# Kernel tuning notes

Measured on AMD Instinct MI355X. Metric: run time of the kernel, lower is better.

## Reference

```python
import jax, jax.numpy as jnp
import numpy as np

N_NODES = 100000
N_EDGES = 3200000
IN_FEAT = 64
OUT_FEAT = 64
NUM_RELS = 16


def setup_inputs() -> dict:
    key = jax.random.key(0)
    k1, k2, k3, k4, k5, k6 = jax.random.split(key, 6)
    h = jax.random.normal(k1, (N_NODES, IN_FEAT), dtype=jnp.float32)
    weight = jax.random.normal(k2, (NUM_RELS, IN_FEAT, OUT_FEAT), dtype=jnp.float32) * 0.1
    norm = jax.random.uniform(k3, (N_EDGES, 1), dtype=jnp.float32)
    src = jax.random.randint(k4, (N_EDGES,), 0, N_NODES, dtype=jnp.int32)
    dst = jax.random.randint(k5, (N_EDGES,), 0, N_NODES, dtype=jnp.int32)
    rel_type = jax.random.randint(k6, (N_EDGES,), 0, NUM_RELS, dtype=jnp.int32)
    return {"h": h, "weight": weight, "norm": norm, "src": src, "dst": dst, "rel_type": rel_type}


def reference(h, weight, norm, src, dst, rel_type):
    # RGCN layer (use_edge_nn=False, num_bases==num_rels, no bias, activation=relu).
    # torch: msg_e = (h[src_e] @ weight[rel_e]) * norm_e ; h_v = relu(sum_{e->v} msg_e)
    # Efficient form: transform every node under every relation once (R is small),
    # then gather per-edge instead of gathering [E, in, out] weight slices.
    n_nodes = h.shape[0]
    transformed = jnp.einsum('nd,rdo->nro', h, weight)          # [N, R, out]
    msg = transformed[src, rel_type] * norm                      # [E, out]
    agg = jax.ops.segment_sum(msg, dst, num_segments=n_nodes)    # [N, out]
    return jax.nn.relu(agg)                                      # dropout is identity in eval
```

## Files before the change

kernel.cpp:

```cpp
#include <hip/hip_runtime.h>

#define N_NODES 100000
#define N_EDGES 3200000
#define FEAT 64
#define NUM_RELS 16
#define CAP 64
#define OVF_CAP 32768
#define RANGES_W 4
#define NODES_PER_W 25000
#define FILL_BLOCKS 1024
#define AGG_BLOCKS (NODES_PER_W / 4)

typedef float f32x4 __attribute__((ext_vector_type(4)));
typedef float f32x16 __attribute__((ext_vector_type(16)));
typedef short s16x8 __attribute__((ext_vector_type(8)));
typedef int   i32x2 __attribute__((ext_vector_type(2)));
typedef int   i32x4 __attribute__((ext_vector_type(4)));

__device__ __forceinline__ unsigned short f32_to_bf16_rne(float x) {
    unsigned int u = __float_as_uint(x);
    unsigned int r = (u + 0x7fffu + ((u >> 16) & 1u)) >> 16;
    return (unsigned short)r;
}
__device__ __forceinline__ float bf16_to_f32(unsigned short s) {
    return __uint_as_float(((unsigned int)s) << 16);
}
__device__ __forceinline__ int t_offset(int s, int r) {
    return ((s >> 4) << 14) | (r << 10) | ((s & 15) << 6);
}

__global__ __launch_bounds__(256) void cvt_h_kernel(const float4* __restrict__ h4,
                                                    ushort4* __restrict__ hb4, int n4)
{
    int i = blockIdx.x * 256 + threadIdx.x;
    if (i < n4) {
        float4 v = h4[i];
        ushort4 o;
        o.x = f32_to_bf16_rne(v.x); o.y = f32_to_bf16_rne(v.y);
        o.z = f32_to_bf16_rne(v.z); o.w = f32_to_bf16_rne(v.w);
        hb4[i] = o;
    }
}

__global__ __launch_bounds__(256) void cvt_w_kernel(const float* __restrict__ W,
                                                    unsigned short* __restrict__ Wt)
{
    int t = blockIdx.x * 256 + threadIdx.x;
    int r = t >> 12, o = (t >> 6) & 63, k = t & 63;
    Wt[t] = f32_to_bf16_rne(W[(r << 12) + (k << 6) + o]);
}

__global__ __launch_bounds__(256) void gemm_T_kernel(
    const unsigned short* __restrict__ hb,
    const unsigned short* __restrict__ Wt,
    unsigned short* __restrict__ T)
{
    __shared__ short lds[4][16][68];
    const int lane  = threadIdx.x & 63;
    const int w     = threadIdx.x >> 6;
    const int row0  = blockIdx.x * 64 + w * 16;
    if (row0 >= N_NODES) return;
    const int q     = lane & 15;
    const int g4    = lane >> 4;

    const unsigned short* ap = hb + ((size_t)(row0 + q) << 6) + (g4 << 3);
    const s16x8 a0 = *reinterpret_cast<const s16x8*>(ap);
    const s16x8 a1 = *reinterpret_cast<const s16x8*>(ap + 32);

    const unsigned short* wbase = Wt + ((size_t)q << 6) + (g4 << 3);
    unsigned short* tb = T + ((size_t)(row0 >> 4) << 14);
    const int nrd = lane >> 4;
    const int c   = lane & 15;

    auto loadB = [&](s16x8* Bf, int r) {
        const unsigned short* wp = wbase + ((size_t)r << 12);
        #pragma unroll
        for (int t = 0; t < 4; ++t)
            #pragma unroll
            for (int kh = 0; kh < 2; ++kh)
                Bf[t * 2 + kh] = *reinterpret_cast<const s16x8*>(wp + (t << 10) + (kh << 5));
    };
    auto compStore = [&](const s16x8* Bf, int rr) {
        f32x4 acc[4] = {f32x4{0,0,0,0}, f32x4{0,0,0,0}, f32x4{0,0,0,0}, f32x4{0,0,0,0}};
        #pragma unroll
        for (int t = 0; t < 4; ++t) {
            acc[t] = __builtin_amdgcn_mfma_f32_16x16x32_bf16(Bf[t*2+0], a0, acc[t], 0, 0, 0);
            acc[t] = __builtin_amdgcn_mfma_f32_16x16x32_bf16(Bf[t*2+1], a1, acc[t], 0, 0, 0);
        }
        #pragma unroll
        for (int t = 0; t < 4; ++t) {
            i32x2 pk;
            pk.x = (int)((unsigned)f32_to_bf16_rne(acc[t][0]) |
                         ((unsigned)f32_to_bf16_rne(acc[t][1]) << 16));
            pk.y = (int)((unsigned)f32_to_bf16_rne(acc[t][2]) |
                         ((unsigned)f32_to_bf16_rne(acc[t][3]) << 16));
            *reinterpret_cast<i32x2*>(&lds[w][q][g4 * 4 + t * 16]) = pk;
        }
        asm volatile("s_waitcnt lgkmcnt(0)" ::: "memory");
        unsigned short* tr = tb + (rr << 10);
        #pragma unroll
        for (int j = 0; j < 4; ++j) {
            const int n = nrd + 4 * j;
            i32x2 v = *reinterpret_cast<const i32x2*>(&lds[w][n][c * 4]);
            *reinterpret_cast<i32x2*>(tr + (n << 6) + (c << 2)) = v;
        }
    };

    s16x8 B0[8], B1[8];
    loadB(B0, 0);
    #pragma unroll
    for (int rp = 0; rp < 16; rp += 2) {
        loadB(B1, rp + 1);
        compStore(B0, rp);
        if (rp + 2 < 16) loadB(B0, rp + 2);
        compStore(B1, rp + 1);
    }
}

__global__ __launch_bounds__(256) void fill_agg_kernel(
    const int* __restrict__ src, const int* __restrict__ dst,
    const int* __restrict__ rel, const float* __restrict__ norm,
    int* __restrict__ cnt, int* __restrict__ ovfc, i32x4* __restrict__ ovf,
    i32x2* __restrict__ payF, const i32x2* __restrict__ payG,
    const unsigned short* __restrict__ T, float* __restrict__ out,
    int fillRange, int aggRange)
{
    const int nFill = (fillRange >= 0) ? FILL_BLOCKS : 0;
    if ((int)blockIdx.x < nFill) {
        const int lo = fillRange * NODES_PER_W, hi = lo + NODES_PER_W;
        for (int e = blockIdx.x * 256 + threadIdx.x; e < N_EDGES; e += nFill * 256) {
            int d = __builtin_nontemporal_load(&dst[e]);
            if (d >= lo && d < hi) {
                int s   = __builtin_nontemporal_load(&src[e]);
                int rl  = __builtin_nontemporal_load(&rel[e]);
                float nv = __builtin_nontemporal_load(&norm[e]);
                int tofs = t_offset(s, rl);
                int pos = atomicAdd(&cnt[d], 1);
                if (pos < CAP) {
                    i32x2 p; p.x = tofs; p.y = __float_as_int(nv);
                    payF[(size_t)(d - lo) * CAP + pos] = p;
                } else {
                    int op = atomicAdd(ovfc, 1);
                    if (op < OVF_CAP) {
                        i32x4 o; o.x = d; o.y = tofs;
                        o.z = __float_as_int(nv); o.w = 0;
                        ovf[op] = o;
                    }
                }
            }
        }
    } else {
        const int b    = blockIdx.x - nFill;
        const int lo   = aggRange * NODES_PER_W;
        const int lane = threadIdx.x & 63;
        const int d    = lo + b * 4 + (threadIdx.x >> 6);

        const int degRaw = __builtin_amdgcn_readfirstlane(cnt[d]);
        const int deg    = min(degRaw, CAP);
        const i32x2* pp  = payG + (size_t)(d - lo) * CAP;

        float acc = 0.f;
        int i = 0;
        for (; i + 4 <= deg; i += 4) {
            i32x2 p0 = __builtin_nontemporal_load(&pp[i]);
            i32x2 p1 = __builtin_nontemporal_load(&pp[i + 1]);
            i32x2 p2 = __builtin_nontemporal_load(&pp[i + 2]);
            i32x2 p3 = __builtin_nontemporal_load(&pp[i + 3]);
            const unsigned short t0 = T[(size_t)(unsigned)p0.x + lane];
            const unsigned short t1 = T[(size_t)(unsigned)p1.x + lane];
            const unsigned short t2 = T[(size_t)(unsigned)p2.x + lane];
            const unsigned short t3 = T[(size_t)(unsigned)p3.x + lane];
            acc = fmaf(__int_as_float(p0.y), bf16_to_f32(t0), acc);
            acc = fmaf(__int_as_float(p1.y), bf16_to_f32(t1), acc);
            acc = fmaf(__int_as_float(p2.y), bf16_to_f32(t2), acc);
            acc = fmaf(__int_as_float(p3.y), bf16_to_f32(t3), acc);
        }
        for (; i < deg; ++i) {
            i32x2 p = __builtin_nontemporal_load(&pp[i]);
            const unsigned short t = T[(size_t)(unsigned)p.x + lane];
            acc = fmaf(__int_as_float(p.y), bf16_to_f32(t), acc);
        }
        if (degRaw > CAP) {
            const int no = min(__builtin_amdgcn_readfirstlane(*ovfc), OVF_CAP);
            for (int j = 0; j < no; ++j) {
                i32x4 o = ovf[j];
                if (o.x == d) {
                    const unsigned short t = T[(size_t)(unsigned)o.y + lane];
                    acc = fmaf(__int_as_float(o.z), bf16_to_f32(t), acc);
                }
            }
        }
        out[((size_t)d << 6) + lane] = fmaxf(acc, 0.f);
    }
}

__global__ __launch_bounds__(256) void rgcn_edge_kernel(
    const float* __restrict__ h, const float* __restrict__ W,
    const float* __restrict__ norm, const int* __restrict__ src,
    const int* __restrict__ dst, const int* __restrict__ rel,
    float* __restrict__ out)
{
    const int lane = threadIdx.x & 63;
    const int w    = threadIdx.x >> 6;
    const int r    = blockIdx.x & 15;
    const int inst = blockIdx.x >> 4;
    const int wavesPerRel = (gridDim.x >> 4) * 4;
    const int wi   = inst * 4 + w;

    float wreg[64];
    const float* Wr = W + (size_t)r * (FEAT * FEAT) + lane;
    #pragma unroll
    for (int d = 0; d < 64; ++d) wreg[d] = Wr[d * 64];

    const int nChunks = N_EDGES / 64;
    for (int c = wi; c < nChunks; c += wavesPerRel) {
        const int base = c * 64;
        unsigned long long m = __ballot(rel[base + lane] == r);
        while (m) {
            const int idx = __ffsll(m) - 1;
            m &= (m - 1);
            const int e = base + idx;
            const int se = __builtin_amdgcn_readfirstlane(src[e]);
            const int de = __builtin_amdgcn_readfirstlane(dst[e]);
            const float nv = __uint_as_float(
                __builtin_amdgcn_readfirstlane(__float_as_uint(norm[e])));
            const float* hp = h + ((size_t)se << 6);
            f32x16 ha, hb2, hc, hd;
            asm volatile(
                "s_load_dwordx16 %0, %4, 0x0\n\ts_load_dwordx16 %1, %4, 0x40\n\t"
                "s_load_dwordx16 %2, %4, 0x80\n\ts_load_dwordx16 %3, %4, 0xc0\n\t"
                "s_waitcnt lgkmcnt(0)"
                : "=&s"(ha), "=&s"(hb2), "=&s"(hc), "=&s"(hd) : "s"(hp));
            float a0 = 0.f, a1 = 0.f, a2 = 0.f, a3 = 0.f;
            #pragma unroll
            for (int j = 0; j < 16; ++j) {
                a0 = fmaf(ha[j], wreg[j], a0);       a1 = fmaf(hb2[j], wreg[16 + j], a1);
                a2 = fmaf(hc[j], wreg[32 + j], a2);  a3 = fmaf(hd[j], wreg[48 + j], a3);
            }
            unsafeAtomicAdd(&out[(size_t)de * FEAT + lane], ((a0 + a1) + (a2 + a3)) * nv);
        }
    }
}

__global__ __launch_bounds__(256) void relu_kernel(float4* __restrict__ out, int n4)
{
    int i = blockIdx.x * 256 + threadIdx.x;
    if (i < n4) {
        float4 v = out[i];
        v.x = fmaxf(v.x, 0.f); v.y = fmaxf(v.y, 0.f);
        v.z = fmaxf(v.z, 0.f); v.w = fmaxf(v.w, 0.f);
        out[i] = v;
    }
}

static inline size_t align256(size_t x) { return (x + 255) & ~(size_t)255; }

extern "C" void kernel_launch(void* const* d_in, const int* in_sizes, int n_in,
                              void* d_out, int out_size, void* d_ws, size_t ws_size,
                              hipStream_t stream)
{
    (void)in_sizes; (void)n_in;

    const float* h    = (const float*)d_in[0];
    const float* W    = (const float*)d_in[1];
    const float* norm = (const float*)d_in[2];
    const int*   src  = (const int*)d_in[3];
    const int*   dst  = (const int*)d_in[4];
    const int*   rel  = (const int*)d_in[5];
    float*       out  = (float*)d_out;

    const size_t szT    = (size_t)N_NODES * NUM_RELS * FEAT * 2;
    const size_t szHb   = (size_t)N_NODES * FEAT * 2;
    const size_t szWt   = (size_t)NUM_RELS * FEAT * FEAT * 2;
    const size_t szCnt  = (size_t)N_NODES * 4;
    const size_t szPayW = (size_t)NODES_PER_W * CAP * 8;
    const size_t szOvf  = (size_t)OVF_CAP * 16;

    const size_t needWin = align256(szT) + align256(szHb) + align256(szWt)
                         + 2 * align256(szPayW) + align256(szCnt) + align256(256)
                         + align256(szOvf);

    const int n4h = N_NODES * FEAT / 4;

    if (ws_size >= needWin) {
        char* ws = (char*)d_ws; size_t off = 0;
        unsigned short* T    = (unsigned short*)(ws + off); off += align256(szT);
        unsigned short* hb   = (unsigned short*)(ws + off); off += align256(szHb);
        unsigned short* Wt   = (unsigned short*)(ws + off); off += align256(szWt);
        i32x2*          pay0 = (i32x2*)         (ws + off); off += align256(szPayW);
        i32x2*          pay1 = (i32x2*)         (ws + off); off += align256(szPayW);
        int*            cnt  = (int*)           (ws + off); off += align256(szCnt);
        int*            ovfc = (int*)           (ws + off); off += align256(256);
        i32x4*          ovf  = (i32x4*)         (ws + off); off += align256(szOvf);

        hipLaunchKernelGGL(cvt_h_kernel, dim3((n4h + 255) / 256), dim3(256), 0, stream,
                           (const float4*)h, (ushort4*)hb, n4h);
        hipLaunchKernelGGL(cvt_w_kernel, dim3(NUM_RELS * FEAT * FEAT / 256), dim3(256),
                           0, stream, W, Wt);
        hipMemsetAsync(cnt, 0, szCnt, stream);
        hipMemsetAsync(ovfc, 0, 256, stream);

        hipLaunchKernelGGL(gemm_T_kernel, dim3((N_NODES + 63) / 64), dim3(256), 0, stream,
                           hb, Wt, T);

        i32x2* win[2] = {pay0, pay1};
        hipLaunchKernelGGL(fill_agg_kernel, dim3(FILL_BLOCKS), dim3(256), 0, stream,
                           src, dst, rel, norm, cnt, ovfc, ovf,
                           win[0], (const i32x2*)nullptr, T, out, 0, -1);
        for (int r = 1; r < RANGES_W; ++r) {
            hipLaunchKernelGGL(fill_agg_kernel, dim3(FILL_BLOCKS + AGG_BLOCKS), dim3(256),
                               0, stream, src, dst, rel, norm, cnt, ovfc, ovf,
                               win[r & 1], win[(r - 1) & 1], T, out, r, r - 1);
        }
        hipLaunchKernelGGL(fill_agg_kernel, dim3(AGG_BLOCKS), dim3(256), 0, stream,
                           src, dst, rel, norm, cnt, ovfc, ovf,
                           (i32x2*)nullptr, win[(RANGES_W - 1) & 1], T, out,
                           -1, RANGES_W - 1);
        return;
    }

    hipMemsetAsync(d_out, 0, (size_t)out_size * sizeof(float), stream);
    hipLaunchKernelGGL(rgcn_edge_kernel, dim3(16 * 128), dim3(256), 0, stream,
                       h, W, norm, src, dst, rel, out);
    const int n4 = out_size / 4;
    hipLaunchKernelGGL(relu_kernel, dim3((n4 + 255) / 256), dim3(256), 0, stream,
                       (float4*)d_out, n4);
}
```

Measured before the change: 434.6 us.

## Fuse GEMM with first-range edge fill and split GEMM across relation groups

```diff
diff --git a/kernel.cpp b/kernel.cpp
--- a/kernel.cpp
+++ b/kernel.cpp
@@ -10,6 +10,8 @@
 #define NODES_PER_W 25000
 #define FILL_BLOCKS 1024
 #define AGG_BLOCKS (NODES_PER_W / 4)
+#define NODE_TILES 1563
+#define NGEMM (NODE_TILES * 4)
 
 typedef float f32x4 __attribute__((ext_vector_type(4)));
 typedef float f32x16 __attribute__((ext_vector_type(16)));
@@ -50,15 +52,47 @@
     Wt[t] = f32_to_bf16_rne(W[(r << 12) + (k << 6) + o]);
 }
 
-__global__ __launch_bounds__(256) void gemm_T_kernel(
+__global__ __launch_bounds__(256) void gemm_fill_kernel(
     const unsigned short* __restrict__ hb,
     const unsigned short* __restrict__ Wt,
-    unsigned short* __restrict__ T)
-{
+    unsigned short* __restrict__ T,
+    const int* __restrict__ src, const int* __restrict__ dst,
+    const int* __restrict__ rel, const float* __restrict__ norm,
+    int* __restrict__ cnt, int* __restrict__ ovfc, i32x4* __restrict__ ovf,
+    i32x2* __restrict__ payF)
+{
+    if ((int)blockIdx.x >= NGEMM) {
+        const int b = blockIdx.x - NGEMM;
+        for (int e = b * 256 + threadIdx.x; e < N_EDGES; e += FILL_BLOCKS * 256) {
+            int d = __builtin_nontemporal_load(&dst[e]);
+            if (d < NODES_PER_W) {
+                int s   = __builtin_nontemporal_load(&src[e]);
+                int rl  = __builtin_nontemporal_load(&rel[e]);
+                float nv = __builtin_nontemporal_load(&norm[e]);
+                int tofs = t_offset(s, rl);
+                int pos = atomicAdd(&cnt[d], 1);
+                if (pos < CAP) {
+                    i32x2 p; p.x = tofs; p.y = __float_as_int(nv);
+                    payF[(size_t)d * CAP + pos] = p;
+                } else {
+                    int op = atomicAdd(ovfc, 1);
+                    if (op < OVF_CAP) {
+                        i32x4 o; o.x = d; o.y = tofs;
+                        o.z = __float_as_int(nv); o.w = 0;
+                        ovf[op] = o;
+                    }
+                }
+            }
+        }
+        return;
+    }
+
     __shared__ short lds[4][16][68];
     const int lane  = threadIdx.x & 63;
     const int w     = threadIdx.x >> 6;
-    const int row0  = blockIdx.x * 64 + w * 16;
+    const int tile  = blockIdx.x >> 2;
+    const int rg    = blockIdx.x & 3;
+    const int row0  = tile * 64 + w * 16;
     if (row0 >= N_NODES) return;
     const int q     = lane & 15;
     const int g4    = lane >> 4;
@@ -106,15 +140,16 @@
         }
     };
 
+    const int r0 = rg * 4;
     s16x8 B0[8], B1[8];
-    loadB(B0, 0);
-    #pragma unroll
-    for (int rp = 0; rp < 16; rp += 2) {
-        loadB(B1, rp + 1);
-        compStore(B0, rp);
-        if (rp + 2 < 16) loadB(B0, rp + 2);
-        compStore(B1, rp + 1);
-    }
+    loadB(B0, r0);
+    loadB(B1, r0 + 1);
+    compStore(B0, r0);
+    loadB(B0, r0 + 2);
+    compStore(B1, r0 + 1);
+    loadB(B1, r0 + 3);
+    compStore(B0, r0 + 2);
+    compStore(B1, r0 + 3);
 }
 
 __global__ __launch_bounds__(256) void fill_agg_kernel(
@@ -300,13 +335,10 @@
         hipMemsetAsync(cnt, 0, szCnt, stream);
         hipMemsetAsync(ovfc, 0, 256, stream);
 
-        hipLaunchKernelGGL(gemm_T_kernel, dim3((N_NODES + 63) / 64), dim3(256), 0, stream,
-                           hb, Wt, T);
+        hipLaunchKernelGGL(gemm_fill_kernel, dim3(NGEMM + FILL_BLOCKS), dim3(256), 0, stream,
+                           hb, Wt, T, src, dst, rel, norm, cnt, ovfc, ovf, pay0);
 
         i32x2* win[2] = {pay0, pay1};
-        hipLaunchKernelGGL(fill_agg_kernel, dim3(FILL_BLOCKS), dim3(256), 0, stream,
-                           src, dst, rel, norm, cnt, ovfc, ovf,
-                           win[0], (const i32x2*)nullptr, T, out, 0, -1);
         for (int r = 1; r < RANGES_W; ++r) {
             hipLaunchKernelGGL(fill_agg_kernel, dim3(FILL_BLOCKS + AGG_BLOCKS), dim3(256),
                                0, stream, src, dst, rel, norm, cnt, ovfc, ovf,
```

Result: faster. 425.4 us (-2.1%).

## Aggregate raw features per relation then apply weights via MFMA per node group

Applied to the files above, without the earlier changes.

```diff
diff --git a/kernel.cpp b/kernel.cpp
--- a/kernel.cpp
+++ b/kernel.cpp
@@ -9,7 +9,9 @@
 #define RANGES_W 4
 #define NODES_PER_W 25000
 #define FILL_BLOCKS 1024
-#define AGG_BLOCKS (NODES_PER_W / 4)
+#define AGG_G 4
+#define AGG_BLOCKS (NODES_PER_W / AGG_G)
+#define HS_STRIDE 1028
 
 typedef float f32x4 __attribute__((ext_vector_type(4)));
 typedef float f32x16 __attribute__((ext_vector_type(16)));
@@ -24,9 +26,6 @@
 }
 __device__ __forceinline__ float bf16_to_f32(unsigned short s) {
     return __uint_as_float(((unsigned int)s) << 16);
-}
-__device__ __forceinline__ int t_offset(int s, int r) {
-    return ((s >> 4) << 14) | (r << 10) | ((s & 15) << 6);
 }
 
 __global__ __launch_bounds__(256) void cvt_h_kernel(const float4* __restrict__ h4,
@@ -50,82 +49,18 @@
     Wt[t] = f32_to_bf16_rne(W[(r << 12) + (k << 6) + o]);
 }
 
-__global__ __launch_bounds__(256) void gemm_T_kernel(
+__global__ __launch_bounds__(256) void fill_agg2_kernel(
     const unsigned short* __restrict__ hb,
     const unsigned short* __restrict__ Wt,
-    unsigned short* __restrict__ T)
-{
-    __shared__ short lds[4][16][68];
-    const int lane  = threadIdx.x & 63;
-    const int w     = threadIdx.x >> 6;
-    const int row0  = blockIdx.x * 64 + w * 16;
-    if (row0 >= N_NODES) return;
-    const int q     = lane & 15;
-    const int g4    = lane >> 4;
-
-    const unsigned short* ap = hb + ((size_t)(row0 + q) << 6) + (g4 << 3);
-    const s16x8 a0 = *reinterpret_cast<const s16x8*>(ap);
-    const s16x8 a1 = *reinterpret_cast<const s16x8*>(ap + 32);
-
-    const unsigned short* wbase = Wt + ((size_t)q << 6) + (g4 << 3);
-    unsigned short* tb = T + ((size_t)(row0 >> 4) << 14);
-    const int nrd = lane >> 4;
-    const int c   = lane & 15;
-
-    auto loadB = [&](s16x8* Bf, int r) {
-        const unsigned short* wp = wbase + ((size_t)r << 12);
-        #pragma unroll
-        for (int t = 0; t < 4; ++t)
-            #pragma unroll
-            for (int kh = 0; kh < 2; ++kh)
-                Bf[t * 2 + kh] = *reinterpret_cast<const s16x8*>(wp + (t << 10) + (kh << 5));
-    };
-    auto compStore = [&](const s16x8* Bf, int rr) {
-        f32x4 acc[4] = {f32x4{0,0,0,0}, f32x4{0,0,0,0}, f32x4{0,0,0,0}, f32x4{0,0,0,0}};
-        #pragma unroll
-        for (int t = 0; t < 4; ++t) {
-            acc[t] = __builtin_amdgcn_mfma_f32_16x16x32_bf16(Bf[t*2+0], a0, acc[t], 0, 0, 0);
-            acc[t] = __builtin_amdgcn_mfma_f32_16x16x32_bf16(Bf[t*2+1], a1, acc[t], 0, 0, 0);
-        }
-        #pragma unroll
-        for (int t = 0; t < 4; ++t) {
-            i32x2 pk;
-            pk.x = (int)((unsigned)f32_to_bf16_rne(acc[t][0]) |
-                         ((unsigned)f32_to_bf16_rne(acc[t][1]) << 16));
-            pk.y = (int)((unsigned)f32_to_bf16_rne(acc[t][2]) |
-                         ((unsigned)f32_to_bf16_rne(acc[t][3]) << 16));
-            *reinterpret_cast<i32x2*>(&lds[w][q][g4 * 4 + t * 16]) = pk;
-        }
-        asm volatile("s_waitcnt lgkmcnt(0)" ::: "memory");
-        unsigned short* tr = tb + (rr << 10);
-        #pragma unroll
-        for (int j = 0; j < 4; ++j) {
-            const int n = nrd + 4 * j;
-            i32x2 v = *reinterpret_cast<const i32x2*>(&lds[w][n][c * 4]);
-            *reinterpret_cast<i32x2*>(tr + (n << 6) + (c << 2)) = v;
-        }
-    };
-
-    s16x8 B0[8], B1[8];
-    loadB(B0, 0);
-    #pragma unroll
-    for (int rp = 0; rp < 16; rp += 2) {
-        loadB(B1, rp + 1);
-        compStore(B0, rp);
-        if (rp + 2 < 16) loadB(B0, rp + 2);
-        compStore(B1, rp + 1);
-    }
-}
-
-__global__ __launch_bounds__(256) void fill_agg_kernel(
     const int* __restrict__ src, const int* __restrict__ dst,
     const int* __restrict__ rel, const float* __restrict__ norm,
     int* __restrict__ cnt, int* __restrict__ ovfc, i32x4* __restrict__ ovf,
     i32x2* __restrict__ payF, const i32x2* __restrict__ payG,
-    const unsigned short* __restrict__ T, float* __restrict__ out,
-    int fillRange, int aggRange)
-{
+    float* __restrict__ out, int fillRange, int aggRange)
+{
+    __shared__ float hsum[AGG_G][HS_STRIDE];
     const int nFill = (fillRange >= 0) ? FILL_BLOCKS : 0;
+
     if ((int)blockIdx.x < nFill) {
         const int lo = fillRange * NODES_PER_W, hi = lo + NODES_PER_W;
         for (int e = blockIdx.x * 256 + threadIdx.x; e < N_EDGES; e += nFill * 256) {
@@ -134,63 +69,109 @@
                 int s   = __builtin_nontemporal_load(&src[e]);
                 int rl  = __builtin_nontemporal_load(&rel[e]);
                 float nv = __builtin_nontemporal_load(&norm[e]);
-                int tofs = t_offset(s, rl);
                 int pos = atomicAdd(&cnt[d], 1);
                 if (pos < CAP) {
-                    i32x2 p; p.x = tofs; p.y = __float_as_int(nv);
+                    i32x2 p; p.x = (s << 4) | rl; p.y = __float_as_int(nv);
                     payF[(size_t)(d - lo) * CAP + pos] = p;
                 } else {
                     int op = atomicAdd(ovfc, 1);
                     if (op < OVF_CAP) {
-                        i32x4 o; o.x = d; o.y = tofs;
+                        i32x4 o; o.x = d; o.y = (s << 4) | rl;
                         o.z = __float_as_int(nv); o.w = 0;
                         ovf[op] = o;
                     }
                 }
             }
         }
-    } else {
-        const int b    = blockIdx.x - nFill;
-        const int lo   = aggRange * NODES_PER_W;
-        const int lane = threadIdx.x & 63;
-        const int d    = lo + b * 4 + (threadIdx.x >> 6);
-
-        const int degRaw = __builtin_amdgcn_readfirstlane(cnt[d]);
-        const int deg    = min(degRaw, CAP);
-        const i32x2* pp  = payG + (size_t)(d - lo) * CAP;
-
-        float acc = 0.f;
-        int i = 0;
-        for (; i + 4 <= deg; i += 4) {
-            i32x2 p0 = __builtin_nontemporal_load(&pp[i]);
-            i32x2 p1 = __builtin_nontemporal_load(&pp[i + 1]);
-            i32x2 p2 = __builtin_nontemporal_load(&pp[i + 2]);
-            i32x2 p3 = __builtin_nontemporal_load(&pp[i + 3]);
-            const unsigned short t0 = T[(size_t)(unsigned)p0.x + lane];
-            const unsigned short t1 = T[(size_t)(unsigned)p1.x + lane];
-            const unsigned short t2 = T[(size_t)(unsigned)p2.x + lane];
-            const unsigned short t3 = T[(size_t)(unsigned)p3.x + lane];
-            acc = fmaf(__int_as_float(p0.y), bf16_to_f32(t0), acc);
-            acc = fmaf(__int_as_float(p1.y), bf16_to_f32(t1), acc);
-            acc = fmaf(__int_as_float(p2.y), bf16_to_f32(t2), acc);
-            acc = fmaf(__int_as_float(p3.y), bf16_to_f32(t3), acc);
-        }
-        for (; i < deg; ++i) {
-            i32x2 p = __builtin_nontemporal_load(&pp[i]);
-            const unsigned short t = T[(size_t)(unsigned)p.x + lane];
-            acc = fmaf(__int_as_float(p.y), bf16_to_f32(t), acc);
-        }
-        if (degRaw > CAP) {
-            const int no = min(__builtin_amdgcn_readfirstlane(*ovfc), OVF_CAP);
-            for (int j = 0; j < no; ++j) {
-                i32x4 o = ovf[j];
-                if (o.x == d) {
-                    const unsigned short t = T[(size_t)(unsigned)o.y + lane];
-                    acc = fmaf(__int_as_float(o.z), bf16_to_f32(t), acc);
+        return;
+    }
+
+    const int b     = blockIdx.x - nFill;
+    const int winLo = aggRange * NODES_PER_W;
+    const int base  = winLo + b * AGG_G;
+    const int lane  = threadIdx.x & 63;
+    const int w     = threadIdx.x >> 6;
+    const int d     = base + w;
+
+    float facc[16];
+    #pragma unroll
+    for (int rr = 0; rr < 16; ++rr) facc[rr] = 0.f;
+
+    const int degRaw = __builtin_amdgcn_readfirstlane(cnt[d]);
+    const int deg    = min(degRaw, CAP);
+    const i32x2* pp  = payG + (size_t)(d - winLo) * CAP;
+
+    for (int i = 0; i < deg; ++i) {
+        i32x2 p = pp[i];
+        const int sx   = __builtin_amdgcn_readfirstlane(p.x);
+        const float nv = __uint_as_float(
+            (unsigned)__builtin_amdgcn_readfirstlane(p.y));
+        const int s = sx >> 4;
+        const int r = sx & 15;
+        const float hv = bf16_to_f32(hb[((size_t)s << 6) + lane]);
+        const float c  = nv * hv;
+        switch (r) {
+            case 0:  facc[0]  += c; break;  case 1:  facc[1]  += c; break;
+            case 2:  facc[2]  += c; break;  case 3:  facc[3]  += c; break;
+            case 4:  facc[4]  += c; break;  case 5:  facc[5]  += c; break;
+            case 6:  facc[6]  += c; break;  case 7:  facc[7]  += c; break;
+            case 8:  facc[8]  += c; break;  case 9:  facc[9]  += c; break;
+            case 10: facc[10] += c; break;  case 11: facc[11] += c; break;
+            case 12: facc[12] += c; break;  case 13: facc[13] += c; break;
+            case 14: facc[14] += c; break;  default: facc[15] += c; break;
+        }
+    }
+    if (degRaw > CAP) {
+        const int no = min(__builtin_amdgcn_readfirstlane(*ovfc), OVF_CAP);
+        for (int j = 0; j < no; ++j) {
+            i32x4 o = ovf[j];
+            if (o.x == d) {
+                const int sx = o.y;
+                const float nv = __uint_as_float((unsigned)o.z);
+                const float hv = bf16_to_f32(hb[((size_t)(sx >> 4) << 6) + lane]);
+                const float c  = nv * hv;
+                switch (sx & 15) {
+                    case 0:  facc[0]  += c; break;  case 1:  facc[1]  += c; break;
+                    case 2:  facc[2]  += c; break;  case 3:  facc[3]  += c; break;
+                    case 4:  facc[4]  += c; break;  case 5:  facc[5]  += c; break;
+                    case 6:  facc[6]  += c; break;  case 7:  facc[7]  += c; break;
+                    case 8:  facc[8]  += c; break;  case 9:  facc[9]  += c; break;
+                    case 10: facc[10] += c; break;  case 11: facc[11] += c; break;
+                    case 12: facc[12] += c; break;  case 13: facc[13] += c; break;
+                    case 14: facc[14] += c; break;  default: facc[15] += c; break;
                 }
             }
         }
-        out[((size_t)d << 6) + lane] = fmaxf(acc, 0.f);
+    }
+    #pragma unroll
+    for (int rr = 0; rr < 16; ++rr)
+        hsum[w][rr * 64 + lane] = facc[rr];
+    __syncthreads();
+
+    const int q  = lane & 15;
+    const int g4 = lane >> 4;
+    f32x4 acc = {0.f, 0.f, 0.f, 0.f};
+    const unsigned short* wb = Wt + ((size_t)(w * 16 + q) << 6) + (g4 << 3);
+    for (int kk = 0; kk < 32; ++kk) {
+        s16x8 af = {0, 0, 0, 0, 0, 0, 0, 0};
+        if (q < AGG_G) {
+            const float* hp = &hsum[q][kk * 32 + g4 * 8];
+            f32x4 u0 = *reinterpret_cast<const f32x4*>(hp);
+            f32x4 u1 = *reinterpret_cast<const f32x4*>(hp + 4);
+            #pragma unroll
+            for (int j = 0; j < 4; ++j) {
+                af[j]     = (short)f32_to_bf16_rne(u0[j]);
+                af[4 + j] = (short)f32_to_bf16_rne(u1[j]);
+            }
+        }
+        s16x8 bf = *reinterpret_cast<const s16x8*>(
+            wb + ((size_t)(kk >> 1) << 12) + ((kk & 1) << 5));
+        acc = __builtin_amdgcn_mfma_f32_16x16x32_bf16(af, bf, acc, 0, 0, 0);
+    }
+    if (g4 == 0) {
+        #pragma unroll
+        for (int rg = 0; rg < 4; ++rg)
+            out[((size_t)(base + rg) << 6) + w * 16 + q] = fmaxf(acc[rg], 0.f);
     }
 }
 
@@ -269,22 +250,19 @@
     const int*   rel  = (const int*)d_in[5];
     float*       out  = (float*)d_out;
 
-    const size_t szT    = (size_t)N_NODES * NUM_RELS * FEAT * 2;
     const size_t szHb   = (size_t)N_NODES * FEAT * 2;
     const size_t szWt   = (size_t)NUM_RELS * FEAT * FEAT * 2;
     const size_t szCnt  = (size_t)N_NODES * 4;
     const size_t szPayW = (size_t)NODES_PER_W * CAP * 8;
     const size_t szOvf  = (size_t)OVF_CAP * 16;
 
-    const size_t needWin = align256(szT) + align256(szHb) + align256(szWt)
-                         + 2 * align256(szPayW) + align256(szCnt) + align256(256)
-                         + align256(szOvf);
+    const size_t need = align256(szHb) + align256(szWt) + 2 * align256(szPayW)
+                      + align256(szCnt) + align256(256) + align256(szOvf);
 
     const int n4h = N_NODES * FEAT / 4;
 
-    if (ws_size >= needWin) {
+    if (ws_size >= need) {
         char* ws = (char*)d_ws; size_t off = 0;
-        unsigned short* T    = (unsigned short*)(ws + off); off += align256(szT);
         unsigned short* hb   = (unsigned short*)(ws + off); off += align256(szHb);
         unsigned short* Wt   = (unsigned short*)(ws + off); off += align256(szWt);
         i32x2*          pay0 = (i32x2*)         (ws + off); off += align256(szPayW);
@@ -300,21 +278,18 @@
         hipMemsetAsync(cnt, 0, szCnt, stream);
         hipMemsetAsync(ovfc, 0, 256, stream);
 
-        hipLaunchKernelGGL(gemm_T_kernel, dim3((N_NODES + 63) / 64), dim3(256), 0, stream,
-                           hb, Wt, T);
-
         i32x2* win[2] = {pay0, pay1};
-        hipLaunchKernelGGL(fill_agg_kernel, dim3(FILL_BLOCKS), dim3(256), 0, stream,
-                           src, dst, rel, norm, cnt, ovfc, ovf,
-                           win[0], (const i32x2*)nullptr, T, out, 0, -1);
+        hipLaunchKernelGGL(fill_agg2_kernel, dim3(FILL_BLOCKS), dim3(256), 0, stream,
+                           hb, Wt, src, dst, rel, norm, cnt, ovfc, ovf,
+                           win[0], (const i32x2*)nullptr, out, 0, -1);
         for (int r = 1; r < RANGES_W; ++r) {
-            hipLaunchKernelGGL(fill_agg_kernel, dim3(FILL_BLOCKS + AGG_BLOCKS), dim3(256),
-                               0, stream, src, dst, rel, norm, cnt, ovfc, ovf,
-                               win[r & 1], win[(r - 1) & 1], T, out, r, r - 1);
-        }
-        hipLaunchKernelGGL(fill_agg_kernel, dim3(AGG_BLOCKS), dim3(256), 0, stream,
-                           src, dst, rel, norm, cnt, ovfc, ovf,
-                           (i32x2*)nullptr, win[(RANGES_W - 1) & 1], T, out,
+            hipLaunchKernelGGL(fill_agg2_kernel, dim3(FILL_BLOCKS + AGG_BLOCKS), dim3(256),
+                               0, stream, hb, Wt, src, dst, rel, norm, cnt, ovfc, ovf,
+                               win[r & 1], win[(r - 1) & 1], out, r, r - 1);
+        }
+        hipLaunchKernelGGL(fill_agg2_kernel, dim3(AGG_BLOCKS), dim3(256), 0, stream,
+                           hb, Wt, src, dst, rel, norm, cnt, ovfc, ovf,
+                           (i32x2*)nullptr, win[(RANGES_W - 1) & 1], out,
                            -1, RANGES_W - 1);
         return;
     }
```

Measured after the change: 785.3 us. 1.81x slower.
